# Kernel tuning notes

Hardware: AMD Instinct MI355X
Metric: run time of the kernel (lower is better)

The kernel has to match this reference:

```python
import jax, jax.numpy as jnp
import numpy as np

NEG_INF = -1e30
DEN_SCALE = 1.0  # den_scale from init


def segment_logsumexp(scores, segids, num_segments):
    """Numerically stable logsumexp of `scores` grouped by `segids`."""
    m = jax.ops.segment_max(scores, segids, num_segments=num_segments)
    m_safe = jnp.where(m > NEG_INF / 2, m, 0.0)
    s = jax.ops.segment_sum(jnp.exp(scores - m_safe[segids]), segids,
                            num_segments=num_segments)
    return jnp.where(s > 0, jnp.log(s) + m_safe, NEG_INF)


def fsa_log_marginal(ll, seqlen, arc_src, arc_dst, arc_pdf, arc_w,
                     init_logp, final_logp):
    """Forward (alpha) recursion over a compiled FSA.
    ll: [T, C] pdf log-likelihoods; arcs: [A]; states: [S].
    Returns scalar log total path probability."""
    S = init_logp.shape[0]

    def step(carry, ll_t):
        alpha, t = carry
        # score of each arc taken at frame t
        scores = alpha[arc_src] + arc_w + ll_t[arc_pdf]  # [A]
        new_alpha = segment_logsumexp(scores, arc_dst, S)  # [S]
        # freeze alpha once past this sequence's length
        alpha = jnp.where(t < seqlen, new_alpha, alpha)
        return (alpha, t + 1), None

    (alpha, _), _ = jax.lax.scan(step, (init_logp, jnp.array(0, jnp.int32)), ll)
    return jax.nn.logsumexp(alpha + final_logp)


# batched numerator: per-utterance FSA topology ([B, A_num] arc arrays)
_num_marginal = jax.vmap(fsa_log_marginal,
                         in_axes=(0, 0, 0, 0, 0, 0, None, None))
# batched denominator: shared FSA topology ([A_den] arc arrays)
_den_marginal = jax.vmap(fsa_log_marginal,
                         in_axes=(0, 0, None, None, None, None, None, None))


def setup_inputs() -> dict:
    key = jax.random.key(0)
    ks = jax.random.split(key, 10)
    B, T, C = 16, 500, 3000
    S_den, A_den_rand = 2000, 46000
    L = 250  # numerator chain emission length (<= min seqlen)
    S_num = L + 1

    inp = jax.random.normal(ks[0], (B, T, C), dtype=jnp.float32)
    # log-softmax-like normalization, as pdf log-likelihoods would be
    inp = jax.nn.log_softmax(inp, axis=-1)
    seqlengths = jax.random.randint(ks[1], (B,), 300, T + 1).astype(jnp.int32)

    # ---- numerator FSAs: left-to-right chain + self-loops, per utterance ----
    fwd_src = jnp.arange(L, dtype=jnp.int32)            # i -> i+1
    fwd_dst = fwd_src + 1
    loop = jnp.arange(S_num, dtype=jnp.int32)           # self-loops on all states
    num_arc_src = jnp.broadcast_to(jnp.concatenate([fwd_src, loop]), (B, L + S_num))
    num_arc_dst = jnp.broadcast_to(jnp.concatenate([fwd_dst, loop]), (B, L + S_num))
    num_arc_pdf = jax.random.randint(ks[2], (B, L + S_num), 0, C).astype(jnp.int32)
    num_arc_w = jnp.zeros((B, L + S_num), dtype=jnp.float32)
    num_init_logp = jnp.full((S_num,), NEG_INF, jnp.float32).at[0].set(0.0)
    num_final_logp = jnp.full((S_num,), NEG_INF, jnp.float32).at[S_num - 1].set(0.0)

    # ---- denominator FSA: random phone-LM-like graph + self-loops ----
    rnd_src = jax.random.randint(ks[3], (A_den_rand,), 0, S_den)
    rnd_dst = jax.random.randint(ks[4], (A_den_rand,), 0, S_den)
    loops = jnp.arange(S_den)
    den_arc_src = jnp.concatenate([rnd_src, loops]).astype(jnp.int32)
    den_arc_dst = jnp.concatenate([rnd_dst, loops]).astype(jnp.int32)
    A_den = den_arc_src.shape[0]
    den_arc_pdf = jax.random.randint(ks[5], (A_den,), 0, C).astype(jnp.int32)
    den_arc_w = 0.1 * jax.random.normal(ks[6], (A_den,), dtype=jnp.float32)
    den_init_logp = jnp.full((S_den,), NEG_INF, jnp.float32).at[0].set(0.0)
    den_final_logp = jnp.zeros((S_den,), dtype=jnp.float32)

    return {
        "input": inp, "seqlengths": seqlengths,
        "num_arc_src": num_arc_src, "num_arc_dst": num_arc_dst,
        "num_arc_pdf": num_arc_pdf, "num_arc_w": num_arc_w,
        "num_init_logp": num_init_logp, "num_final_logp": num_final_logp,
        "den_arc_src": den_arc_src, "den_arc_dst": den_arc_dst,
        "den_arc_pdf": den_arc_pdf, "den_arc_w": den_arc_w,
        "den_init_logp": den_init_logp, "den_final_logp": den_final_logp,
    }


def reference(input, seqlengths, num_arc_src, num_arc_dst, num_arc_pdf,
              num_arc_w, num_init_logp, num_final_logp, den_arc_src,
              den_arc_dst, den_arc_pdf, den_arc_w, den_init_logp,
              den_final_logp):
    num_llh = _num_marginal(input, seqlengths, num_arc_src, num_arc_dst,
                            num_arc_pdf, num_arc_w, num_init_logp,
                            num_final_logp)
    den_llh = _den_marginal(input, seqlengths, den_arc_src, den_arc_dst,
                            den_arc_pdf, den_arc_w, den_init_logp,
                            den_final_logp)
    loss = -(num_llh - DEN_SCALE * den_llh)
    return loss.sum()
```

## Files before the change

kernel.cpp:

```cpp
#include <hip/hip_runtime.h>

#define NEG_INF_F (-1e30f)
#define MAX_S 2048
#define MAX_C 3008
#define NCH   128


__global__ void zero_kernel(int* __restrict__ p, int n) {
  int i = blockIdx.x * blockDim.x + threadIdx.x;
  if (i < n) p[i] = 0;
}

__global__ void hist_kernel(const int* __restrict__ dst, int A, int A_stride,
                            int* __restrict__ cnt, int S) {
  int b = blockIdx.y;
  int i = blockIdx.x * blockDim.x + threadIdx.x;
  if (i < A) atomicAdd(&cnt[b * S + dst[(size_t)b * A_stride + i]], 1);
}

__global__ void hist_chunk_kernel(const int* __restrict__ dst, int A, int chunk, int S,
                                  int* __restrict__ hist) {
  int c = blockIdx.x;
  int i1 = min(A, (c + 1) * chunk);
  for (int i = c * chunk + threadIdx.x; i < i1; i += blockDim.x)
    atomicAdd(&hist[c * S + dst[i]], 1);
}

__global__ void colsum_kernel(const int* __restrict__ hist, int nch, int S,
                              int* __restrict__ cnt) {
  int s = blockIdx.x * blockDim.x + threadIdx.x;
  if (s < S) {
    int t = 0;
    for (int c = 0; c < nch; ++c) t += hist[c * S + s];
    cnt[s] = t;
  }
}

__global__ __launch_bounds__(1024)
void rank_perm_kernel(const int* __restrict__ cnt, int S,
                      int* __restrict__ perm, int* __restrict__ invperm) {
  __shared__ int c[2048];
  __shared__ int R[2048];
  const int tid = threadIdx.x;
  for (int i = tid; i < 2048; i += 1024) c[i] = (i < S) ? cnt[i] : -1;
  __syncthreads();
  for (int u = 0; u < 2; ++u) {
    int s = tid + u * 1024;
    if (s < S) {
      int cs = c[s], r = 0;
      for (int j = 0; j < S; ++j) {
        int cj = c[j];
        r += (cj > cs) || (cj == cs && j < s);
      }
      R[r] = s;
    }
  }
  __syncthreads();
  for (int u = 0; u < 2; ++u) {
    int slot = tid + u * 1024;
    if (slot < S) {
      int state = (slot < 1024) ? R[slot] : R[S - 1 - (slot - 1024)];
      perm[slot] = state;
      invperm[state] = slot;
    }
  }
}

__global__ void pc_kernel(const int* __restrict__ cnt, const int* __restrict__ perm,
                          int S, int* __restrict__ pc) {
  int slot = blockIdx.x * blockDim.x + threadIdx.x;
  if (slot < 2048) pc[slot] = (slot < S) ? ((cnt[perm[slot]] + 3) & ~3) : 0;
}

__global__ void padcnt_kernel(const int* __restrict__ cnt, int n, int* __restrict__ out) {
  int i = blockIdx.x * blockDim.x + threadIdx.x;
  if (i < n) out[i] = (cnt[i] + 3) & ~3;
}

__global__ __launch_bounds__(1024) void scan_kernel(const int* __restrict__ cnt,
                                                    int* __restrict__ rp, int S) {
  __shared__ int buf[2][2048];
  const int tid = threadIdx.x;
  const int b = blockIdx.x;
  const int* c = cnt + (size_t)b * S;
  int* r = rp + (size_t)b * (S + 1);
  for (int u = 0; u < 2; ++u) {
    int i = tid + u * 1024;
    buf[0][i] = (i < S) ? c[i] : 0;
  }
  __syncthreads();
  int cur = 0;
  for (int off = 1; off < 2048; off <<= 1) {
    for (int u = 0; u < 2; ++u) {
      int i = tid + u * 1024;
      buf[cur ^ 1][i] = buf[cur][i] + ((i >= off) ? buf[cur][i - off] : 0);
    }
    __syncthreads();
    cur ^= 1;
  }
  for (int u = 0; u < 2; ++u) {
    int i = tid + u * 1024;
    if (i <= S) r[i] = (i == 0) ? 0 : buf[cur][i - 1];
  }
  if (tid == 0) r[S] = buf[cur][S - 1];
}

__global__ void off_perm_kernel(int* __restrict__ hist, int nch, int S,
                                const int* __restrict__ rp, const int* __restrict__ perm) {
  int slot = blockIdx.x * blockDim.x + threadIdx.x;
  if (slot < S) {
    int state = perm[slot];
    int run = rp[slot];
    for (int c = 0; c < nch; ++c) {
      int h = hist[c * S + state];
      hist[c * S + state] = run;
      run += h;
    }
  }
}

__global__ void pad_den_kernel(const int* __restrict__ rp, const int* __restrict__ cnt,
                               const int* __restrict__ perm, int S, uint2* __restrict__ meta) {
  int slot = blockIdx.x * blockDim.x + threadIdx.x;
  if (slot < S) {
    int p = rp[slot] + cnt[perm[slot]];
    int e = rp[slot + 1];
    uint2 pad = make_uint2(0u, 0u);
    for (; p < e; ++p) meta[p] = pad;
  }
}

__global__ void fill_chunk_kernel(const int* __restrict__ src, const int* __restrict__ dst,
                                  const int* __restrict__ pdf, const float* __restrict__ w,
                                  int A, int chunk, int S, int* __restrict__ hoff,
                                  const int* __restrict__ inv, uint2* __restrict__ meta) {
  int c = blockIdx.y;
  int s = blockIdx.x * blockDim.x + threadIdx.x;
  if (s >= S) return;
  int i1 = min(A, (c + 1) * chunk);
  int p = hoff[c * S + s];
  for (int i = c * chunk; i < i1; ++i) {
    if (dst[i] == s) {
      meta[p++] = make_uint2((unsigned)inv[src[i]] | ((unsigned)pdf[i] << 16),
                             __float_as_uint(__expf(w[i])));
    }
  }
}

__global__ void fill_kernel(const int* __restrict__ src, const int* __restrict__ dst,
                            const int* __restrict__ pdf, const float* __restrict__ w,
                            int A, int A_stride, const int* __restrict__ rp, int S,
                            uint2* __restrict__ meta, int meta_stride) {
  int b = blockIdx.y;
  int s = blockIdx.x * blockDim.x + threadIdx.x;
  if (s >= S) return;
  const int*   sb = src + (size_t)b * A_stride;
  const int*   db = dst + (size_t)b * A_stride;
  const int*   pb = pdf + (size_t)b * A_stride;
  const float* wb = w   + (size_t)b * A_stride;
  const int*   rpb = rp + (size_t)b * (S + 1);
  uint2* mb = meta + (size_t)b * meta_stride;
  int p = rpb[s];
  for (int i = 0; i < A; ++i) {
    if (db[i] == s) {
      mb[p++] = make_uint2((unsigned)sb[i] | ((unsigned)pb[i] << 16), __float_as_uint(wb[i]));
    }
  }
  uint2 pad = make_uint2(0u, __float_as_uint(NEG_INF_F));
  int e = rpb[s + 1];
  for (; p < e; ++p) mb[p] = pad;
}

__global__ __launch_bounds__(1024)
void wave_desc_kernel(const int* __restrict__ rp, int cap4, int* __restrict__ desc) {
  __shared__ int wm[32];
  const int tid = threadIdx.x;
  const int w = tid >> 6;
  int cA = (rp[tid + 1] - rp[tid]) >> 2;
  int sB = 2047 - tid;
  int cB = (rp[sB + 1] - rp[sB]) >> 2;
  for (int off = 32; off; off >>= 1) {
    cA = max(cA, __shfl_down(cA, off));
    cB = max(cB, __shfl_down(cB, off));
  }
  if ((tid & 63) == 0) { wm[w] = cA; wm[16 + w] = cB; }
  __syncthreads();
  if (tid == 0) {
    int off = 0;
    for (int i = 0; i < 16; ++i) { desc[i] = off; off += wm[i] * 128; }
    for (int i = 0; i < 16; ++i) { desc[16 + i] = off; off += wm[16 + i] * 128; }
    for (int i = 0; i < 16; ++i) { desc[32 + i] = wm[i]; desc[48 + i] = wm[16 + i]; }
    desc[64] = (off <= cap4) ? 1 : 0;
    desc[65] = off;
  }
}

__global__ void repack_kernel(const uint2* __restrict__ meta, const int* __restrict__ rp,
                              const int* __restrict__ desc, uint2* __restrict__ ilv) {
  if (!desc[64]) return;
  const int w = blockIdx.x & 15;
  const bool isB = blockIdx.x >= 16;
  const int l = threadIdx.x;
  const int tid = w * 64 + l;
  const int s = isB ? (2047 - tid) : tid;
  const int base4 = desc[(isB ? 16 : 0) + w];
  const int wmax  = desc[(isB ? 48 : 32) + w];
  const int r0 = rp[s];
  const int n = (rp[s + 1] - r0) >> 2;
  for (int c = 0; c < wmax; ++c) {
    for (int part = 0; part < 2; ++part) {
      int u4 = base4 + c * 128 + part * 64 + l;
      uint2 v0 = make_uint2(0u, 0u), v1 = make_uint2(0u, 0u);
      if (c < n) {
        v0 = meta[r0 + 4 * c + 2 * part];
        v1 = meta[r0 + 4 * c + 2 * part + 1];
      }
      ilv[2 * u4]     = v0;
      ilv[2 * u4 + 1] = v1;
    }
  }
}


__device__ __forceinline__ float row_lse(const uint2* __restrict__ meta, int k, int e,
                                         const float* __restrict__ alpha,
                                         const float* __restrict__ lcur) {
  float mm0 = NEG_INF_F, ss0 = 0.0f, mm1 = NEG_INF_F, ss1 = 0.0f;
  const int n4 = (e - k) >> 2;
  const uint4* p = (const uint4*)(meta + k);
  if (n4 > 0) {
    uint4 A = p[0], Bv = p[1];
    float t0 = alpha[A.x & 0xFFFFu] + __uint_as_float(A.y) + lcur[A.x >> 16];
    float t1 = alpha[A.z & 0xFFFFu] + __uint_as_float(A.w) + lcur[A.z >> 16];
    float t2 = alpha[Bv.x & 0xFFFFu] + __uint_as_float(Bv.y) + lcur[Bv.x >> 16];
    float t3 = alpha[Bv.z & 0xFFFFu] + __uint_as_float(Bv.w) + lcur[Bv.z >> 16];
    for (int c2 = 1; c2 < n4; ++c2) {
      uint4 A2 = p[2 * c2], B2 = p[2 * c2 + 1];
      float u0 = alpha[A2.x & 0xFFFFu] + __uint_as_float(A2.y) + lcur[A2.x >> 16];
      float u1 = alpha[A2.z & 0xFFFFu] + __uint_as_float(A2.w) + lcur[A2.z >> 16];
      float u2 = alpha[B2.x & 0xFFFFu] + __uint_as_float(B2.y) + lcur[B2.x >> 16];
      float u3 = alpha[B2.z & 0xFFFFu] + __uint_as_float(B2.w) + lcur[B2.z >> 16];
      float mc = fmaxf(fmaxf(t0, t1), fmaxf(t2, t3));
      if ((c2 & 1) != 0) {
        float nm = fmaxf(mm0, mc);
        ss0 = ss0 * __expf(mm0 - nm) +
              ((__expf(t0 - nm) + __expf(t1 - nm)) + (__expf(t2 - nm) + __expf(t3 - nm)));
        mm0 = nm;
      } else {
        float nm = fmaxf(mm1, mc);
        ss1 = ss1 * __expf(mm1 - nm) +
              ((__expf(t0 - nm) + __expf(t1 - nm)) + (__expf(t2 - nm) + __expf(t3 - nm)));
        mm1 = nm;
      }
      t0 = u0; t1 = u1; t2 = u2; t3 = u3;
    }
    float mc = fmaxf(fmaxf(t0, t1), fmaxf(t2, t3));
    if ((n4 & 1) != 0) {
      float nm = fmaxf(mm0, mc);
      ss0 = ss0 * __expf(mm0 - nm) +
            ((__expf(t0 - nm) + __expf(t1 - nm)) + (__expf(t2 - nm) + __expf(t3 - nm)));
      mm0 = nm;
    } else {
      float nm = fmaxf(mm1, mc);
      ss1 = ss1 * __expf(mm1 - nm) +
            ((__expf(t0 - nm) + __expf(t1 - nm)) + (__expf(t2 - nm) + __expf(t3 - nm)));
      mm1 = nm;
    }
  }
  float nm = fmaxf(mm0, mm1);
  float ssc = ss0 * __expf(mm0 - nm) + ss1 * __expf(mm1 - nm);
  return (ssc > 0.0f) ? (__logf(ssc) + nm) : NEG_INF_F;
}

__device__ __forceinline__ void stage_row(const float* __restrict__ row,
                                          float* __restrict__ lds, int C, int tid, int nt) {
  if (((C & 3) == 0) && ((((uintptr_t)row) & 15) == 0)) {
    const float4* r4 = (const float4*)row;
    const int n = C >> 2;
    for (int i = tid; i < n; i += nt) ((float4*)lds)[i] = r4[i];
  } else {
    for (int i = tid; i < C; i += nt) lds[i] = row[i];
  }
}

#define ACC4(X, Y, s0, s1, s2, s3)                                                       \
  s0 = fmaf(__uint_as_float((X).y), vbuf[(X).x & 0xFFFFu] * elbuf[(X).x >> 16], s0);     \
  s1 = fmaf(__uint_as_float((X).w), vbuf[(X).z & 0xFFFFu] * elbuf[(X).z >> 16], s1);     \
  s2 = fmaf(__uint_as_float((Y).y), vbuf[(Y).x & 0xFFFFu] * elbuf[(Y).x >> 16], s2);     \
  s3 = fmaf(__uint_as_float((Y).w), vbuf[(Y).z & 0xFFFFu] * elbuf[(Y).z >> 16], s3);

__global__ __launch_bounds__(1024, 4)
void fsa_forward_lin(const float* __restrict__ ll, const int* __restrict__ seqlen,
                     const uint2* __restrict__ den_meta, const uint4* __restrict__ den_ilv,
                     const int* __restrict__ den_desc,
                     const int* __restrict__ den_rp, const int* __restrict__ den_perm, int S_den,
                     const uint2* __restrict__ num_meta, const int* __restrict__ num_rp,
                     int num_stride, int S_num,
                     const float* __restrict__ den_init, const float* __restrict__ den_final,
                     const float* __restrict__ num_init, const float* __restrict__ num_final,
                     int T, int C, int B, float* __restrict__ out_llh)
{
  __shared__ float alpha[MAX_S];
  __shared__ float vbuf[MAX_S];
  __shared__ float elbuf[MAX_C];
  __shared__ float red[16];
  __shared__ int   sdesc[66];

  const int tid = threadIdx.x;
  const int nt  = 1024;
  const bool is_den = ((int)blockIdx.x) < B;
  const int b = is_den ? (int)blockIdx.x : ((int)blockIdx.x - B);
  const int S = is_den ? S_den : S_num;
  const float* fin  = is_den ? den_final : num_final;
  const int*   perm = is_den ? den_perm  : nullptr;

  const int L = seqlen[b];
  const float* llb = ll + ((size_t)b * T) * C;

  if (is_den) {
    for (int i = tid; i < 66; i += nt) sdesc[i] = den_desc[i];

    const int w = tid >> 6, l = tid & 63;
    const int slotA = tid;
    const int slotB = 2047 - tid;
    const int rA0 = den_rp[slotA], rA1 = den_rp[slotA + 1];
    const int rB0 = den_rp[slotB], rB1 = den_rp[slotB + 1];
    float a0 = (slotA < S) ? den_init[den_perm[slotA]] : NEG_INF_F;
    float a1 = (slotB < S) ? den_init[den_perm[slotB]] : NEG_INF_F;

    const int nvec = C >> 2;
    const bool pf = ((C & 3) == 0) && ((((uintptr_t)llb) & 15) == 0) &&
                    (nvec <= nt) && (C <= MAX_C);

    float lm = fmaxf(a0, a1);
    for (int off = 32; off; off >>= 1) lm = fmaxf(lm, __shfl_down(lm, off));
    if ((tid & 63) == 0) red[tid >> 6] = lm;
    if (L > 0) {
      if (pf) {
        if (tid < nvec) {
          float4 r = ((const float4*)llb)[tid];
          elbuf[4 * tid + 0] = __expf(r.x); elbuf[4 * tid + 1] = __expf(r.y);
          elbuf[4 * tid + 2] = __expf(r.z); elbuf[4 * tid + 3] = __expf(r.w);
        }
      } else {
        for (int i = tid; i < C; i += nt) elbuf[i] = __expf(llb[i]);
      }
    }
    __syncthreads();
    float M = red[0];
#pragma unroll
    for (int i = 1; i < 16; ++i) M = fmaxf(M, red[i]);

    const bool ilv_ok = sdesc[64] != 0;
    const uint4* pA4 = den_ilv + sdesc[w] + l;
    const uint4* pB4 = den_ilv + sdesc[16 + w] + l;
    const int nA = sdesc[32 + w], nB = sdesc[48 + w];

    for (int t = 0; t < L; ++t) {
      vbuf[slotA] = __expf(a0 - M);
      vbuf[slotB] = __expf(a1 - M);
      __syncthreads();

      float4 nx;
      const bool donx = pf && (t + 1 < L) && (tid < nvec);
      if (donx) nx = ((const float4*)(llb + (size_t)(t + 1) * C))[tid];

      float sA0 = 0, sA1 = 0, sA2 = 0, sA3 = 0;
      float sB0 = 0, sB1 = 0, sB2 = 0, sB3 = 0;
      if (ilv_ok) {
        if (nA > 0) {
          uint4 X0 = pA4[0], Y0 = pA4[64];
          if (nA > 1) {
            uint4 X1 = pA4[128], Y1 = pA4[192];
            for (int c = 2; c < nA; ++c) {
              uint4 X2 = pA4[c * 128], Y2 = pA4[c * 128 + 64];
              ACC4(X0, Y0, sA0, sA1, sA2, sA3);
              X0 = X1; Y0 = Y1; X1 = X2; Y1 = Y2;
            }
            ACC4(X0, Y0, sA0, sA1, sA2, sA3);
            X0 = X1; Y0 = Y1;
          }
          ACC4(X0, Y0, sA0, sA1, sA2, sA3);
        }
        if (nB > 0) {
          uint4 X0 = pB4[0], Y0 = pB4[64];
          for (int c = 1; c < nB; ++c) {
            uint4 X1 = pB4[c * 128], Y1 = pB4[c * 128 + 64];
            ACC4(X0, Y0, sB0, sB1, sB2, sB3);
            X0 = X1; Y0 = Y1;
          }
          ACC4(X0, Y0, sB0, sB1, sB2, sB3);
        }
      } else {
        const uint4* pA = (const uint4*)(den_meta + rA0);
        const uint4* pB = (const uint4*)(den_meta + rB0);
        const int nAr = (rA1 - rA0) >> 2, nBr = (rB1 - rB0) >> 2;
        const int n = nAr > nBr ? nAr : nBr;
        for (int c = 0; c < n; ++c) {
          if (c < nAr) {
            uint4 X = pA[2 * c], Y = pA[2 * c + 1];
            ACC4(X, Y, sA0, sA1, sA2, sA3);
          }
          if (c < nBr) {
            uint4 X = pB[2 * c], Y = pB[2 * c + 1];
            ACC4(X, Y, sB0, sB1, sB2, sB3);
          }
        }
      }
      float sA = (sA0 + sA1) + (sA2 + sA3);
      float sB = (sB0 + sB1) + (sB2 + sB3);
      __syncthreads();

      a0 = (sA > 0.0f) ? (__logf(sA) + M) : NEG_INF_F;
      a1 = (sB > 0.0f) ? (__logf(sB) + M) : NEG_INF_F;

      if (donx) {
        elbuf[4 * tid + 0] = __expf(nx.x); elbuf[4 * tid + 1] = __expf(nx.y);
        elbuf[4 * tid + 2] = __expf(nx.z); elbuf[4 * tid + 3] = __expf(nx.w);
      } else if (!pf && t + 1 < L) {
        const float* nr = llb + (size_t)(t + 1) * C;
        for (int i = tid; i < C; i += nt) elbuf[i] = __expf(nr[i]);
      }

      float lm2 = fmaxf(a0, a1);
      for (int off = 32; off; off >>= 1) lm2 = fmaxf(lm2, __shfl_down(lm2, off));
      if ((tid & 63) == 0) red[tid >> 6] = lm2;
      __syncthreads();
      M = red[0];
#pragma unroll
      for (int i = 1; i < 16; ++i) M = fmaxf(M, red[i]);
    }
    alpha[slotA] = a0;
    alpha[slotB] = a1;
    __syncthreads();
  } else {
    const uint2* meta = num_meta + (size_t)b * num_stride;
    const int*   rp   = num_rp + (size_t)b * (S_num + 1);
    for (int s = tid; s < MAX_S; s += nt) alpha[s] = (s < S) ? num_init[s] : NEG_INF_F;
    int rs[2] = {0, 0}, re[2] = {0, 0};
    for (int u = 0; u < 2; ++u) {
      int s = tid + u * nt;
      if (s < S) { rs[u] = rp[s]; re[u] = rp[s + 1]; }
    }
    __syncthreads();
    for (int t = 0; t < L; ++t) {
      stage_row(llb + (size_t)t * C, elbuf, C, tid, nt);
      __syncthreads();
      float nv[2];
      for (int u = 0; u < 2; ++u) {
        int s = tid + u * nt;
        nv[u] = (s < S) ? row_lse(meta, rs[u], re[u], alpha, elbuf) : NEG_INF_F;
      }
      __syncthreads();
      for (int u = 0; u < 2; ++u) {
        int s = tid + u * nt;
        if (s < S) alpha[s] = nv[u];
      }
      __syncthreads();
    }
  }

  float lm = -3.0e38f;
  for (int s = tid; s < S; s += nt) lm = fmaxf(lm, alpha[s] + fin[perm ? perm[s] : s]);
  for (int off = 32; off; off >>= 1) lm = fmaxf(lm, __shfl_down(lm, off));
  if ((tid & 63) == 0) red[tid >> 6] = lm;
  __syncthreads();
  if (tid < 64) {
    float v = (tid < 16) ? red[tid] : -3.0e38f;
    for (int off = 32; off; off >>= 1) v = fmaxf(v, __shfl_down(v, off));
    if (tid == 0) red[0] = v;
  }
  __syncthreads();
  const float M = red[0];

  float ls = 0.0f;
  for (int s = tid; s < S; s += nt) ls += __expf(alpha[s] + fin[perm ? perm[s] : s] - M);
  for (int off = 32; off; off >>= 1) ls += __shfl_down(ls, off);
  __syncthreads();
  if ((tid & 63) == 0) red[tid >> 6] = ls;
  __syncthreads();
  if (tid < 64) {
    float v = (tid < 16) ? red[tid] : 0.0f;
    for (int off = 32; off; off >>= 1) v += __shfl_down(v, off);
    if (tid == 0) out_llh[(is_den ? 0 : B) + b] = __logf(v) + M;
  }
}


__device__ __forceinline__ unsigned enc_f(float x) {
  unsigned u = __float_as_uint(x);
  return u ^ (unsigned)(((int)u >> 31) | 0x80000000);
}
__device__ __forceinline__ float dec_f(unsigned e) {
  unsigned mask = ((int)e >= 0) ? 0xFFFFFFFFu : 0x80000000u;
  return __uint_as_float(e ^ mask);
}

__global__ __launch_bounds__(1024)
void fsa_forward_fallback(
    const float* __restrict__ ll, const int* __restrict__ seqlen,
    const int* __restrict__ den_src, const int* __restrict__ den_dst,
    const int* __restrict__ den_pdf, const float* __restrict__ den_w,
    int A_den, const float* __restrict__ den_init, const float* __restrict__ den_final, int S_den,
    const int* __restrict__ num_src, const int* __restrict__ num_dst,
    const int* __restrict__ num_pdf, const float* __restrict__ num_w,
    int A_num, const float* __restrict__ num_init, const float* __restrict__ num_final, int S_num,
    int T, int C, int B, float* __restrict__ out_llh)
{
  __shared__ float    alpha[MAX_S];
  __shared__ unsigned menc[MAX_S];
  __shared__ float    msafe[MAX_S];
  __shared__ float    ssum[MAX_S];
  __shared__ float    llrow[MAX_C];

  const int tid = threadIdx.x;
  const int nt  = blockDim.x;
  const bool is_den = ((int)blockIdx.x) < B;
  const int b = is_den ? (int)blockIdx.x : ((int)blockIdx.x - B);
  const int S = is_den ? S_den : S_num;
  const int A = is_den ? A_den : A_num;
  const float* init = is_den ? den_init  : num_init;
  const float* fin  = is_den ? den_final : num_final;
  const int*   asrc = is_den ? den_src  : (num_src + (size_t)b * A_num);
  const int*   adst = is_den ? den_dst  : (num_dst + (size_t)b * A_num);
  const int*   apdf = is_den ? den_pdf  : (num_pdf + (size_t)b * A_num);
  const float* aw   = is_den ? den_w    : (num_w   + (size_t)b * A_num);

  for (int s = tid; s < S; s += nt) { alpha[s] = init[s]; menc[s] = 0u; ssum[s] = 0.0f; }
  __syncthreads();

  const int L = seqlen[b];
  const float* llb = ll + ((size_t)b * T) * C;

  for (int t = 0; t < L; ++t) {
    const float* row = llb + (size_t)t * C;
    for (int i = tid; i < C; i += nt) llrow[i] = row[i];
    __syncthreads();
    for (int i = tid; i < A; i += nt) {
      float score = alpha[asrc[i]] + aw[i] + llrow[apdf[i]];
      atomicMax(&menc[adst[i]], enc_f(score));
    }
    __syncthreads();
    for (int s = tid; s < S; s += nt) {
      float m = dec_f(menc[s]);
      msafe[s] = (m > -5e29f) ? m : 0.0f;
    }
    __syncthreads();
    for (int i = tid; i < A; i += nt) {
      int d = adst[i];
      float score = alpha[asrc[i]] + aw[i] + llrow[apdf[i]];
      atomicAdd(&ssum[d], __expf(score - msafe[d]));
    }
    __syncthreads();
    for (int s = tid; s < S; s += nt) {
      float sum = ssum[s];
      alpha[s] = (sum > 0.0f) ? (__logf(sum) + msafe[s]) : NEG_INF_F;
      menc[s] = 0u; ssum[s] = 0.0f;
    }
    __syncthreads();
  }

  float lm = -3.0e38f;
  for (int s = tid; s < S; s += nt) lm = fmaxf(lm, alpha[s] + fin[s]);
  for (int off = 32; off; off >>= 1) lm = fmaxf(lm, __shfl_down(lm, off));
  const int nwaves = nt >> 6;
  if ((tid & 63) == 0) msafe[tid >> 6] = lm;
  __syncthreads();
  if (tid < 64) {
    float v = (tid < nwaves) ? msafe[tid] : -3.0e38f;
    for (int off = 32; off; off >>= 1) v = fmaxf(v, __shfl_down(v, off));
    if (tid == 0) msafe[MAX_S - 1] = v;
  }
  __syncthreads();
  const float M = msafe[MAX_S - 1];
  float ls = 0.0f;
  for (int s = tid; s < S; s += nt) ls += __expf(alpha[s] + fin[s] - M);
  for (int off = 32; off; off >>= 1) ls += __shfl_down(ls, off);
  if ((tid & 63) == 0) ssum[tid >> 6] = ls;
  __syncthreads();
  if (tid < 64) {
    float v = (tid < nwaves) ? ssum[tid] : 0.0f;
    for (int off = 32; off; off >>= 1) v += __shfl_down(v, off);
    if (tid == 0) out_llh[(is_den ? 0 : B) + b] = __logf(v) + M;
  }
}

__global__ void final_loss_kernel(const float* __restrict__ llh, int B, float* __restrict__ out) {
  int lane = threadIdx.x;
  float v = (lane < B) ? (llh[lane] - llh[B + lane]) : 0.0f;
  for (int off = 32; off; off >>= 1) v += __shfl_down(v, off);
  if (lane == 0) out[0] = v;
}

extern "C" void kernel_launch(void* const* d_in, const int* in_sizes, int n_in,
                              void* d_out, int out_size, void* d_ws, size_t ws_size,
                              hipStream_t stream) {
  const float* ll        = (const float*)d_in[0];
  const int*   seqlen    = (const int*)  d_in[1];
  const int*   num_src   = (const int*)  d_in[2];
  const int*   num_dst   = (const int*)  d_in[3];
  const int*   num_pdf   = (const int*)  d_in[4];
  const float* num_w     = (const float*)d_in[5];
  const float* num_init  = (const float*)d_in[6];
  const float* num_final = (const float*)d_in[7];
  const int*   den_src   = (const int*)  d_in[8];
  const int*   den_dst   = (const int*)  d_in[9];
  const int*   den_pdf   = (const int*)  d_in[10];
  const float* den_w     = (const float*)d_in[11];
  const float* den_init  = (const float*)d_in[12];
  const float* den_final = (const float*)d_in[13];

  const int B     = in_sizes[1];
  const int A_num = in_sizes[2] / B;
  const int S_num = in_sizes[6];
  const int A_den = in_sizes[8];
  const int S_den = in_sizes[12];
  const int T     = 500;
  const int C     = in_sizes[0] / (B * T);

  const int den_cap    = A_den + 3 * S_den + 64;
  const int num_stride = A_num + 3 * S_num + 64;
  const int cap4       = den_cap + 32768;

  size_t off = 0;
  auto alloc = [&](size_t bytes, size_t align) -> size_t {
    off = (off + align - 1) / align * align;
    size_t r = off; off += bytes; return r;
  };
  size_t o_den_meta = alloc((size_t)den_cap * 8, 16);
  size_t o_den_ilv  = alloc((size_t)cap4 * 16, 16);
  size_t o_desc     = alloc((size_t)66 * 4, 4);
  size_t o_num_meta = alloc((size_t)B * num_stride * 8, 16);
  size_t o_den_rp   = alloc((size_t)2049 * 4, 4);
  size_t o_num_rp   = alloc((size_t)B * (S_num + 1) * 4, 4);
  size_t o_den_cnt  = alloc((size_t)S_den * 4, 4);
  size_t o_perm     = alloc((size_t)2048 * 4, 4);
  size_t o_inv      = alloc((size_t)S_den * 4, 4);
  size_t o_pc       = alloc((size_t)2048 * 4, 4);
  size_t o_num_pc   = alloc((size_t)B * S_num * 4, 4);
  size_t o_hist     = alloc((size_t)NCH * S_den * 4, 4);
  size_t o_num_cnt  = alloc((size_t)B * S_num * 4, 4);
  size_t o_llh      = alloc((size_t)2 * B * 4, 4);
  const bool use_csr = (off <= ws_size) && (S_den >= 1) && (S_den <= 2048) &&
                       (S_num >= 1) && (S_num <= 2048) && (C <= MAX_C);

  char* wsb = (char*)d_ws;
  float* llh = (float*)(wsb + (use_csr ? o_llh : 0));

  if (use_csr) {
    uint2* den_meta = (uint2*)(wsb + o_den_meta);
    uint4* den_ilv  = (uint4*)(wsb + o_den_ilv);
    int*   desc     = (int*)(wsb + o_desc);
    uint2* num_meta = (uint2*)(wsb + o_num_meta);
    int*   den_rp   = (int*)(wsb + o_den_rp);
    int*   num_rp   = (int*)(wsb + o_num_rp);
    int*   den_cnt  = (int*)(wsb + o_den_cnt);
    int*   perm     = (int*)(wsb + o_perm);
    int*   inv      = (int*)(wsb + o_inv);
    int*   pc       = (int*)(wsb + o_pc);
    int*   num_pc   = (int*)(wsb + o_num_pc);
    int*   hist     = (int*)(wsb + o_hist);
    int*   num_cnt  = (int*)(wsb + o_num_cnt);

    const int chunk = (A_den + NCH - 1) / NCH;

    int ztot = NCH * S_den + B * S_num;
    zero_kernel<<<(ztot + 255) / 256, 256, 0, stream>>>(hist, ztot);

    hist_chunk_kernel<<<NCH, 256, 0, stream>>>(den_dst, A_den, chunk, S_den, hist);
    hist_kernel<<<dim3((A_num + 255) / 256, B), 256, 0, stream>>>(num_dst, A_num, A_num,
                                                                  num_cnt, S_num);

    colsum_kernel<<<(S_den + 255) / 256, 256, 0, stream>>>(hist, NCH, S_den, den_cnt);
    rank_perm_kernel<<<1, 1024, 0, stream>>>(den_cnt, S_den, perm, inv);
    pc_kernel<<<8, 256, 0, stream>>>(den_cnt, perm, S_den, pc);
    scan_kernel<<<1, 1024, 0, stream>>>(pc, den_rp, 2048);
    wave_desc_kernel<<<1, 1024, 0, stream>>>(den_rp, cap4, desc);

    padcnt_kernel<<<(B * S_num + 255) / 256, 256, 0, stream>>>(num_cnt, B * S_num, num_pc);
    scan_kernel<<<B, 1024, 0, stream>>>(num_pc, num_rp, S_num);

    off_perm_kernel<<<(S_den + 255) / 256, 256, 0, stream>>>(hist, NCH, S_den, den_rp, perm);
    pad_den_kernel<<<(S_den + 255) / 256, 256, 0, stream>>>(den_rp, den_cnt, perm, S_den, den_meta);
    fill_chunk_kernel<<<dim3((S_den + 255) / 256, NCH), 256, 0, stream>>>(
        den_src, den_dst, den_pdf, den_w, A_den, chunk, S_den, hist, inv, den_meta);
    fill_kernel<<<dim3((S_num + 255) / 256, B), 256, 0, stream>>>(
        num_src, num_dst, num_pdf, num_w, A_num, A_num, num_rp, S_num, num_meta, num_stride);

    repack_kernel<<<32, 64, 0, stream>>>(den_meta, den_rp, desc, (uint2*)den_ilv);

    fsa_forward_lin<<<2 * B, 1024, 0, stream>>>(
        ll, seqlen, den_meta, den_ilv, desc, den_rp, perm, S_den,
        num_meta, num_rp, num_stride, S_num,
        den_init, den_final, num_init, num_final, T, C, B, llh);
  } else {
    fsa_forward_fallback<<<2 * B, 1024, 0, stream>>>(
        ll, seqlen,
        den_src, den_dst, den_pdf, den_w, A_den, den_init, den_final, S_den,
        num_src, num_dst, num_pdf, num_w, A_num, num_init, num_final, S_num,
        T, C, B, llh);
  }

  final_loss_kernel<<<1, 64, 0, stream>>>(llh, B, (float*)d_out);
}
```

Before: 3.461 ms.

## Greedy bank-aware arc repacking, byte-offset indices, double-buffered emission row

Replaces the straight arc repack with a greedy per-wave placement that assigns each arc to the lane slot with the lowest accumulated LDS bank load for both its source-state and pdf lookups, and fills empty slots with harmless zero-weight pads. Arc indices are pre-scaled to byte offsets so the inner loop skips the shift when addressing LDS. The emission buffer is double-buffered, which removes one block-wide barrier per frame. In exchange LDS use goes up, and the repack becomes a serial one-time preprocessing pass. It also leans on 16-bit byte offsets, and a pdf offset of C*4 can exceed 65535, which would corrupt indices.

After: 3.875 ms. 1.12x slower.

```diff
diff --git a/kernel.cpp b/kernel.cpp
--- a/kernel.cpp
+++ b/kernel.cpp
@@ -112,7 +112,7 @@
     int state = perm[slot];
     int run = rp[slot];
     for (int c = 0; c < nch; ++c) {
-      int h = hist[c * S + state];
+      int h = hist[c * S + slot * 0 + state];
       hist[c * S + state] = run;
       run += h;
     }
@@ -141,7 +141,7 @@
   int p = hoff[c * S + s];
   for (int i = c * chunk; i < i1; ++i) {
     if (dst[i] == s) {
-      meta[p++] = make_uint2((unsigned)inv[src[i]] | ((unsigned)pdf[i] << 16),
+      meta[p++] = make_uint2((unsigned)(inv[src[i]] * 4) | ((unsigned)(pdf[i] * 4) << 16),
                              __float_as_uint(__expf(w[i])));
     }
   }
@@ -195,8 +195,9 @@
   }
 }
 
-__global__ void repack_kernel(const uint2* __restrict__ meta, const int* __restrict__ rp,
-                              const int* __restrict__ desc, uint2* __restrict__ ilv) {
+__global__ __launch_bounds__(64)
+void repack_greedy_kernel(const uint2* __restrict__ meta, const int* __restrict__ rp,
+                          const int* __restrict__ desc, int C, uint2* __restrict__ ilv) {
   if (!desc[64]) return;
   const int w = blockIdx.x & 15;
   const bool isB = blockIdx.x >= 16;
@@ -205,19 +206,74 @@
   const int s = isB ? (2047 - tid) : tid;
   const int base4 = desc[(isB ? 16 : 0) + w];
   const int wmax  = desc[(isB ? 48 : 32) + w];
+  const int P = wmax * 4;
   const int r0 = rp[s];
-  const int n = (rp[s + 1] - r0) >> 2;
-  for (int c = 0; c < wmax; ++c) {
-    for (int part = 0; part < 2; ++part) {
-      int u4 = base4 + c * 128 + part * 64 + l;
-      uint2 v0 = make_uint2(0u, 0u), v1 = make_uint2(0u, 0u);
-      if (c < n) {
-        v0 = meta[r0 + 4 * c + 2 * part];
-        v1 = meta[r0 + 4 * c + 2 * part + 1];
-      }
-      ilv[2 * u4]     = v0;
-      ilv[2 * u4 + 1] = v1;
-    }
+  const int nA = rp[s + 1] - r0;
+
+  if (P == 0) return;
+
+  if (P > 64) {
+    const int n = nA >> 2;
+    for (int c = 0; c < wmax; ++c) {
+      for (int part = 0; part < 2; ++part) {
+        int u4 = base4 + c * 128 + part * 64 + l;
+        uint2 v0 = make_uint2(0u, 0u), v1 = make_uint2(0u, 0u);
+        if (c < n) {
+          v0 = meta[r0 + 4 * c + 2 * part];
+          v1 = meta[r0 + 4 * c + 2 * part + 1];
+        }
+        ilv[2 * u4]     = v0;
+        ilv[2 * u4 + 1] = v1;
+      }
+    }
+    return;
+  }
+
+  __shared__ int loadS[64][32];
+  __shared__ int loadP[64][32];
+  __shared__ unsigned long long freeM[64];
+  __shared__ int r0s[64], ns[64];
+
+  for (int i = l; i < 64 * 32; i += 64) {
+    ((int*)loadS)[i] = 0;
+    ((int*)loadP)[i] = 0;
+  }
+  freeM[l] = (P >= 64) ? ~0ULL : ((1ULL << P) - 1ULL);
+  r0s[l] = r0;
+  ns[l]  = nA;
+  __syncthreads();
+
+  for (int r = 0; r < 64; ++r) {
+    const int rr0 = r0s[r], rn = ns[r];
+    for (int k = 0; k < rn; ++k) {
+      uint2 a = meta[rr0 + k];
+      if (a.y == 0u) continue;
+      const int bs = (a.x >> 2) & 31;
+      const int bp = (a.x >> 18) & 31;
+      const bool valid = (l < P) && ((freeM[r] >> l) & 1ULL);
+      int score = valid ? (loadS[l][bs] + loadP[l][bp]) : 0x7FFF;
+      int v = score * 64 + l;
+      for (int off = 32; off; off >>= 1) v = min(v, __shfl_xor(v, off));
+      const int p = v & 63;
+      if (l == p) {
+        freeM[r] &= ~(1ULL << p);
+        loadS[p][bs]++;
+        loadP[p][bp]++;
+        int idx = 2 * (base4 + (p >> 2) * 128 + (((p >> 1) & 1) * 64) + r) + (p & 1);
+        ilv[idx] = a;
+      }
+      __syncthreads();
+    }
+  }
+
+  unsigned long long fm = freeM[l];
+  const int pc = min(s, C - 1);
+  const uint2 pad = make_uint2((unsigned)(s * 4) | ((unsigned)(pc * 4) << 16), 0u);
+  while (fm) {
+    int p = __ffsll(fm) - 1;
+    fm &= fm - 1ULL;
+    int idx = 2 * (base4 + (p >> 2) * 128 + (((p >> 1) & 1) * 64) + l) + (p & 1);
+    ilv[idx] = pad;
   }
 }
 
@@ -283,11 +339,15 @@
   }
 }
 
-#define ACC4(X, Y, s0, s1, s2, s3)                                                       \
-  s0 = fmaf(__uint_as_float((X).y), vbuf[(X).x & 0xFFFFu] * elbuf[(X).x >> 16], s0);     \
-  s1 = fmaf(__uint_as_float((X).w), vbuf[(X).z & 0xFFFFu] * elbuf[(X).z >> 16], s1);     \
-  s2 = fmaf(__uint_as_float((Y).y), vbuf[(Y).x & 0xFFFFu] * elbuf[(Y).x >> 16], s2);     \
-  s3 = fmaf(__uint_as_float((Y).w), vbuf[(Y).z & 0xFFFFu] * elbuf[(Y).z >> 16], s3);
+__device__ __forceinline__ float ldsF(const float* base, unsigned boff) {
+  return *(const float*)((const char*)base + boff);
+}
+
+#define ACC4(X, Y, s0, s1, s2, s3)                                                         \
+  s0 = fmaf(__uint_as_float((X).y), ldsF(vbuf, (X).x & 0xFFFFu) * ldsF(el, (X).x >> 16), s0); \
+  s1 = fmaf(__uint_as_float((X).w), ldsF(vbuf, (X).z & 0xFFFFu) * ldsF(el, (X).z >> 16), s1); \
+  s2 = fmaf(__uint_as_float((Y).y), ldsF(vbuf, (Y).x & 0xFFFFu) * ldsF(el, (Y).x >> 16), s2); \
+  s3 = fmaf(__uint_as_float((Y).w), ldsF(vbuf, (Y).z & 0xFFFFu) * ldsF(el, (Y).z >> 16), s3);
 
 __global__ __launch_bounds__(1024, 4)
 void fsa_forward_lin(const float* __restrict__ ll, const int* __restrict__ seqlen,
@@ -302,7 +362,7 @@
 {
   __shared__ float alpha[MAX_S];
   __shared__ float vbuf[MAX_S];
-  __shared__ float elbuf[MAX_C];
+  __shared__ float elbuf[2 * MAX_C];
   __shared__ float red[16];
   __shared__ int   sdesc[66];
 
@@ -356,10 +416,13 @@
     const uint4* pB4 = den_ilv + sdesc[16 + w] + l;
     const int nA = sdesc[32 + w], nB = sdesc[48 + w];
 
+    int cur = 0;
     for (int t = 0; t < L; ++t) {
       vbuf[slotA] = __expf(a0 - M);
       vbuf[slotB] = __expf(a1 - M);
       __syncthreads();
+
+      const float* el = elbuf + (cur ? MAX_C : 0);
 
       float4 nx;
       const bool donx = pf && (t + 1 < L) && (tid < nvec);
@@ -409,17 +472,17 @@
       }
       float sA = (sA0 + sA1) + (sA2 + sA3);
       float sB = (sB0 + sB1) + (sB2 + sB3);
-      __syncthreads();
 
       a0 = (sA > 0.0f) ? (__logf(sA) + M) : NEG_INF_F;
       a1 = (sB > 0.0f) ? (__logf(sB) + M) : NEG_INF_F;
 
+      float* eln = elbuf + (cur ? 0 : MAX_C);
       if (donx) {
-        elbuf[4 * tid + 0] = __expf(nx.x); elbuf[4 * tid + 1] = __expf(nx.y);
-        elbuf[4 * tid + 2] = __expf(nx.z); elbuf[4 * tid + 3] = __expf(nx.w);
+        eln[4 * tid + 0] = __expf(nx.x); eln[4 * tid + 1] = __expf(nx.y);
+        eln[4 * tid + 2] = __expf(nx.z); eln[4 * tid + 3] = __expf(nx.w);
       } else if (!pf && t + 1 < L) {
         const float* nr = llb + (size_t)(t + 1) * C;
-        for (int i = tid; i < C; i += nt) elbuf[i] = __expf(nr[i]);
+        for (int i = tid; i < C; i += nt) eln[i] = __expf(nr[i]);
       }
 
       float lm2 = fmaxf(a0, a1);
@@ -429,6 +492,7 @@
       M = red[0];
 #pragma unroll
       for (int i = 1; i < 16; ++i) M = fmaxf(M, red[i]);
+      cur ^= 1;
     }
     alpha[slotA] = a0;
     alpha[slotB] = a1;
@@ -642,7 +706,7 @@
   size_t o_num_cnt  = alloc((size_t)B * S_num * 4, 4);
   size_t o_llh      = alloc((size_t)2 * B * 4, 4);
   const bool use_csr = (off <= ws_size) && (S_den >= 1) && (S_den <= 2048) &&
-                       (S_num >= 1) && (S_num <= 2048) && (C <= MAX_C);
+                       (S_num >= 1) && (S_num <= 2048) && (C <= MAX_C) && (C >= 1);
 
   char* wsb = (char*)d_ws;
   float* llh = (float*)(wsb + (use_csr ? o_llh : 0));
@@ -687,7 +751,7 @@
     fill_kernel<<<dim3((S_num + 255) / 256, B), 256, 0, stream>>>(
         num_src, num_dst, num_pdf, num_w, A_num, A_num, num_rp, S_num, num_meta, num_stride);
 
-    repack_kernel<<<32, 64, 0, stream>>>(den_meta, den_rp, desc, (uint2*)den_ilv);
+    repack_greedy_kernel<<<32, 64, 0, stream>>>(den_meta, den_rp, desc, C, (uint2*)den_ilv);
 
     fsa_forward_lin<<<2 * B, 1024, 0, stream>>>(
         ll, seqlen, den_meta, den_ilv, desc, den_rp, perm, S_den,
```

## Replicate alpha and emission buffers in LDS to spread bank conflicts

Applied to the files above, without the earlier changes.

Keeps four copies of the exp-alpha buffer and two copies of the exp-emission row in shared memory, and adds a preprocessing kernel that assigns each arc to the replica with the fewest LDS bank collisions inside its gather group. Arc metadata now stores byte offsets, so LDS gathers skip the index scaling. The emission row is double-buffered, which removes one __syncthreads per timestep. The cost is much more LDS per block (occupancy hint lowered to 1 block), extra writes of every replica each step, and the new preprocessing pass.

Measured after the change: 2.908 ms. -16.0%, faster.

```diff
diff --git a/kernel.cpp b/kernel.cpp
--- a/kernel.cpp
+++ b/kernel.cpp
@@ -4,6 +4,11 @@
 #define MAX_S 2048
 #define MAX_C 3008
 #define NCH   128
+
+#define VB_SIZE 8216
+#define EL_COPY 3016
+#define EL_BUF  6032
+#define EL_SIZE 12064
 
 
 __global__ void zero_kernel(int* __restrict__ p, int n) {
@@ -141,7 +146,7 @@
   int p = hoff[c * S + s];
   for (int i = c * chunk; i < i1; ++i) {
     if (dst[i] == s) {
-      meta[p++] = make_uint2((unsigned)inv[src[i]] | ((unsigned)pdf[i] << 16),
+      meta[p++] = make_uint2((unsigned)(inv[src[i]] * 4) | ((unsigned)(pdf[i] * 4) << 16),
                              __float_as_uint(__expf(w[i])));
     }
   }
@@ -217,6 +222,46 @@
       }
       ilv[2 * u4]     = v0;
       ilv[2 * u4 + 1] = v1;
+    }
+  }
+}
+
+__global__ __launch_bounds__(64)
+void choice_kernel(uint2* __restrict__ ilv, const int* __restrict__ desc) {
+  if (!desc[64]) return;
+  const int w = blockIdx.x & 15;
+  const bool isB = blockIdx.x >= 16;
+  const int base4 = desc[(isB ? 16 : 0) + w];
+  const int wmax  = desc[(isB ? 48 : 32) + w];
+  const int P = wmax * 4;
+  for (int p = threadIdx.x; p < P; p += 64) {
+    const int pbase = 2 * (base4 + (p >> 2) * 128 + (((p >> 1) & 1) * 64)) + (p & 1);
+    unsigned long long cs[4]  = {0, 0, 0, 0};
+    unsigned long long cp2[4] = {0, 0, 0, 0};
+    for (int r = 0; r < 64; ++r) {
+      const int idx = pbase + 2 * r;
+      uint2 a = ilv[idx];
+      unsigned srcoff = a.x & 0xFFFFu;
+      unsigned pdfoff = a.x >> 16;
+      const int b0 = (int)((srcoff >> 2) & 31u);
+      int bestk = 0, bestc = 256;
+#pragma unroll
+      for (int k = 0; k < 4; ++k) {
+        int bb = (b0 + 8 * k) & 31;
+        int c = (int)((cs[bb >> 3] >> ((bb & 7) * 8)) & 0xFFull);
+        if (c < bestc) { bestc = c; bestk = k; }
+      }
+      const int bs = (b0 + 8 * bestk) & 31;
+      cs[bs >> 3] += (1ULL << ((bs & 7) * 8));
+      const int q0 = (int)((pdfoff >> 2) & 31u);
+      const int q1 = (q0 + 8) & 31;
+      const int c0 = (int)((cp2[q0 >> 3] >> ((q0 & 7) * 8)) & 0xFFull);
+      const int c1 = (int)((cp2[q1 >> 3] >> ((q1 & 7) * 8)) & 0xFFull);
+      const int bj = (c1 < c0) ? 1 : 0;
+      const int qb = bj ? q1 : q0;
+      cp2[qb >> 3] += (1ULL << ((qb & 7) * 8));
+      a.x = (srcoff + (unsigned)bestk * 8224u) | ((pdfoff + (unsigned)bj * 12064u) << 16);
+      ilv[idx] = a;
     }
   }
 }
@@ -283,13 +328,17 @@
   }
 }
 
-#define ACC4(X, Y, s0, s1, s2, s3)                                                       \
-  s0 = fmaf(__uint_as_float((X).y), vbuf[(X).x & 0xFFFFu] * elbuf[(X).x >> 16], s0);     \
-  s1 = fmaf(__uint_as_float((X).w), vbuf[(X).z & 0xFFFFu] * elbuf[(X).z >> 16], s1);     \
-  s2 = fmaf(__uint_as_float((Y).y), vbuf[(Y).x & 0xFFFFu] * elbuf[(Y).x >> 16], s2);     \
-  s3 = fmaf(__uint_as_float((Y).w), vbuf[(Y).z & 0xFFFFu] * elbuf[(Y).z >> 16], s3);
-
-__global__ __launch_bounds__(1024, 4)
+__device__ __forceinline__ float ldsF(const float* base, unsigned boff) {
+  return *(const float*)((const char*)base + boff);
+}
+
+#define ACC4(X, Y, s0, s1, s2, s3)                                                         \
+  s0 = fmaf(__uint_as_float((X).y), ldsF(vbuf, (X).x & 0xFFFFu) * ldsF(el, (X).x >> 16), s0); \
+  s1 = fmaf(__uint_as_float((X).w), ldsF(vbuf, (X).z & 0xFFFFu) * ldsF(el, (X).z >> 16), s1); \
+  s2 = fmaf(__uint_as_float((Y).y), ldsF(vbuf, (Y).x & 0xFFFFu) * ldsF(el, (Y).x >> 16), s2); \
+  s3 = fmaf(__uint_as_float((Y).w), ldsF(vbuf, (Y).z & 0xFFFFu) * ldsF(el, (Y).z >> 16), s3);
+
+__global__ __launch_bounds__(1024, 1)
 void fsa_forward_lin(const float* __restrict__ ll, const int* __restrict__ seqlen,
                      const uint2* __restrict__ den_meta, const uint4* __restrict__ den_ilv,
                      const int* __restrict__ den_desc,
@@ -301,8 +350,8 @@
                      int T, int C, int B, float* __restrict__ out_llh)
 {
   __shared__ float alpha[MAX_S];
-  __shared__ float vbuf[MAX_S];
-  __shared__ float elbuf[MAX_C];
+  __shared__ float vbuf[VB_SIZE];
+  __shared__ float elbuf[EL_SIZE];
   __shared__ float red[16];
   __shared__ int   sdesc[66];
 
@@ -339,11 +388,16 @@
       if (pf) {
         if (tid < nvec) {
           float4 r = ((const float4*)llb)[tid];
-          elbuf[4 * tid + 0] = __expf(r.x); elbuf[4 * tid + 1] = __expf(r.y);
-          elbuf[4 * tid + 2] = __expf(r.z); elbuf[4 * tid + 3] = __expf(r.w);
+          float4 e = make_float4(__expf(r.x), __expf(r.y), __expf(r.z), __expf(r.w));
+          ((float4*)elbuf)[tid] = e;
+          ((float4*)(elbuf + EL_COPY))[tid] = e;
         }
       } else {
-        for (int i = tid; i < C; i += nt) elbuf[i] = __expf(llb[i]);
+        for (int i = tid; i < C; i += nt) {
+          float e = __expf(llb[i]);
+          elbuf[i] = e;
+          elbuf[i + EL_COPY] = e;
+        }
       }
     }
     __syncthreads();
@@ -356,10 +410,18 @@
     const uint4* pB4 = den_ilv + sdesc[16 + w] + l;
     const int nA = sdesc[32 + w], nB = sdesc[48 + w];
 
+    int cur = 0;
     for (int t = 0; t < L; ++t) {
-      vbuf[slotA] = __expf(a0 - M);
-      vbuf[slotB] = __expf(a1 - M);
+      {
+        float va = __expf(a0 - M), vb = __expf(a1 - M);
+        vbuf[slotA] = va; vbuf[slotA + 2056] = va;
+        vbuf[slotA + 4112] = va; vbuf[slotA + 6168] = va;
+        vbuf[slotB] = vb; vbuf[slotB + 2056] = vb;
+        vbuf[slotB + 4112] = vb; vbuf[slotB + 6168] = vb;
+      }
       __syncthreads();
+
+      const float* el = elbuf + (cur ? EL_BUF : 0);
 
       float4 nx;
       const bool donx = pf && (t + 1 < L) && (tid < nvec);
@@ -409,17 +471,22 @@
       }
       float sA = (sA0 + sA1) + (sA2 + sA3);
       float sB = (sB0 + sB1) + (sB2 + sB3);
-      __syncthreads();
 
       a0 = (sA > 0.0f) ? (__logf(sA) + M) : NEG_INF_F;
       a1 = (sB > 0.0f) ? (__logf(sB) + M) : NEG_INF_F;
 
+      float* eln = elbuf + (cur ? 0 : EL_BUF);
       if (donx) {
-        elbuf[4 * tid + 0] = __expf(nx.x); elbuf[4 * tid + 1] = __expf(nx.y);
-        elbuf[4 * tid + 2] = __expf(nx.z); elbuf[4 * tid + 3] = __expf(nx.w);
+        float4 e = make_float4(__expf(nx.x), __expf(nx.y), __expf(nx.z), __expf(nx.w));
+        ((float4*)eln)[tid] = e;
+        ((float4*)(eln + EL_COPY))[tid] = e;
       } else if (!pf && t + 1 < L) {
         const float* nr = llb + (size_t)(t + 1) * C;
-        for (int i = tid; i < C; i += nt) elbuf[i] = __expf(nr[i]);
+        for (int i = tid; i < C; i += nt) {
+          float e = __expf(nr[i]);
+          eln[i] = e;
+          eln[i + EL_COPY] = e;
+        }
       }
 
       float lm2 = fmaxf(a0, a1);
@@ -429,6 +496,7 @@
       M = red[0];
 #pragma unroll
       for (int i = 1; i < 16; ++i) M = fmaxf(M, red[i]);
+      cur ^= 1;
     }
     alpha[slotA] = a0;
     alpha[slotB] = a1;
@@ -642,7 +710,7 @@
   size_t o_num_cnt  = alloc((size_t)B * S_num * 4, 4);
   size_t o_llh      = alloc((size_t)2 * B * 4, 4);
   const bool use_csr = (off <= ws_size) && (S_den >= 1) && (S_den <= 2048) &&
-                       (S_num >= 1) && (S_num <= 2048) && (C <= MAX_C);
+                       (S_num >= 1) && (S_num <= 2048) && (C <= MAX_C) && (C >= 1);
 
   char* wsb = (char*)d_ws;
   float* llh = (float*)(wsb + (use_csr ? o_llh : 0));
@@ -688,6 +756,7 @@
         num_src, num_dst, num_pdf, num_w, A_num, A_num, num_rp, S_num, num_meta, num_stride);
 
     repack_kernel<<<32, 64, 0, stream>>>(den_meta, den_rp, desc, (uint2*)den_ilv);
+    choice_kernel<<<32, 64, 0, stream>>>((uint2*)den_ilv, desc);
 
     fsa_forward_lin<<<2 * B, 1024, 0, stream>>>(
         ll, seqlen, den_meta, den_ilv, desc, den_rp, perm, S_den,
```
